# Kernel optimization log

Measured on AMD Instinct MI355X. Metric: run time of the kernel, lower is better.

## Reference

```python
import jax, jax.numpy as jnp
import numpy as np
from math import comb

K = 10
N_NODES = 100000
NUM_FEATURES = 512
HIDDEN = 256
NUM_CLASSES = 64
N_EDGES = 3200000


def setup_inputs() -> dict:
    key = jax.random.key(0)
    k = jax.random.split(key, 8)
    x = jax.random.normal(k[0], (N_NODES, NUM_FEATURES), dtype=jnp.float32)
    src = jax.random.randint(k[1], (N_EDGES,), 0, N_NODES, dtype=jnp.int32)
    dst = jax.random.randint(k[2], (N_EDGES,), 0, N_NODES, dtype=jnp.int32)
    # symmetrize so the sym-normalized Laplacian is well-defined (undirected graph)
    src2 = jnp.concatenate([src, dst])
    dst2 = jnp.concatenate([dst, src])
    edge_index = jnp.stack([src2, dst2], axis=0)  # [2, 2E]
    s1 = 1.0 / np.sqrt(NUM_FEATURES)
    s2 = 1.0 / np.sqrt(HIDDEN)
    W1 = jax.random.uniform(k[3], (NUM_FEATURES, HIDDEN), jnp.float32, -s1, s1)
    b1 = jax.random.uniform(k[4], (HIDDEN,), jnp.float32, -s1, s1)
    W2 = jax.random.uniform(k[5], (HIDDEN, NUM_CLASSES), jnp.float32, -s2, s2)
    b2 = jax.random.uniform(k[6], (NUM_CLASSES,), jnp.float32, -s2, s2)
    temp = jnp.ones((K + 1,), dtype=jnp.float32)  # reset_parameters fills with 1
    return {"x": x, "edge_index": edge_index, "W1": W1, "b1": b1, "W2": W2, "b2": b2, "temp": temp}


def bern_prop(h, src, dst, temp, num_nodes):
    # sym-normalized adjacency weights: w = d^{-1/2}[src] * d^{-1/2}[dst]
    deg = jax.ops.segment_sum(jnp.ones_like(src, dtype=h.dtype), src, num_segments=num_nodes)
    dis = jnp.where(deg > 0, jax.lax.rsqrt(jnp.maximum(deg, 1e-30)), 0.0)
    w = dis[src] * dis[dst]  # [E]

    def adj(v):  # A_hat @ v via gather + scatter-add (source_to_target flow)
        return jax.ops.segment_sum(w[:, None] * v[src], dst, num_segments=num_nodes)

    TEMP = jax.nn.relu(temp)
    coef = np.array([comb(K, i) / 2.0 ** K for i in range(K + 1)], dtype=np.float32)

    tmp = [h]
    for _ in range(K):  # (2I - L) h = h + A_hat h
        h = h + adj(h)
        tmp.append(h)
    out = coef[0] * TEMP[0] * tmp[K]
    for i in range(K):
        y = tmp[K - i - 1]
        for _ in range(i + 1):  # L y = y - A_hat y
            y = y - adj(y)
        out = out + coef[i + 1] * TEMP[i + 1] * y
    return out


def reference(x, edge_index, W1, b1, W2, b2, temp):
    # eval mode: dropout is identity
    h = jax.nn.relu(x @ W1 + b1)
    h = h @ W2 + b2  # [N, num_classes]
    src, dst = edge_index[0], edge_index[1]
    h = bern_prop(h, src, dst, temp, x.shape[0])
    return jax.nn.log_softmax(h, axis=1)
```

## Files before the change

### kernel.cpp

```cpp
#include <hip/hip_runtime.h>
#include <hip/hip_bf16.h>
#include <hip/hip_cooperative_groups.h>
#include <math.h>


#define KORD 10

namespace cg = cooperative_groups;

typedef __attribute__((ext_vector_type(8))) short bf16x8;
typedef __attribute__((ext_vector_type(4))) float f32x4;

typedef __attribute__((address_space(1))) const unsigned int* gas_t;
typedef __attribute__((address_space(3))) unsigned int* las_t;

static __device__ __forceinline__ void gll16(const void* g, void* l) {
    __builtin_amdgcn_global_load_lds((gas_t)g, (las_t)l, 16, 0, 0);
}

static __device__ __forceinline__ ushort f2bf(float f) {
    unsigned u = __float_as_uint(f);
    unsigned r = (u + 0x7fffu + ((u >> 16) & 1u)) >> 16;
    return (ushort)r;
}
static __device__ __forceinline__ float bf2f(ushort h) {
    return __uint_as_float(((unsigned)h) << 16);
}
static __device__ __forceinline__ uint pk2t(float a, float b) {
    return (__float_as_uint(a) >> 16) | (__float_as_uint(b) & 0xffff0000u);
}
static __device__ __forceinline__ bf16x8 mk8(uint a, uint b, uint c, uint d) {
    union { uint4 u; bf16x8 v; } x;
    x.u = make_uint4(a, b, c, d);
    return x.v;
}

__global__ void prep_all(const float* __restrict__ temp,
                         const float* __restrict__ W1, const float* __restrict__ W2,
                         float* __restrict__ acoef, int* __restrict__ flags,
                         ushort* __restrict__ w1b,
                         ushort* __restrict__ w2h, ushort* __restrict__ w2l)
{
    int tid = blockIdx.x * 256 + threadIdx.x;
    if (tid == 0) {
        int C[KORD + 1][KORD + 1];
        for (int n = 0; n <= KORD; ++n) {
            for (int k = 0; k <= KORD; ++k) C[n][k] = 0;
            C[n][0] = 1;
            for (int k = 1; k <= n; ++k)
                C[n][k] = C[n - 1][k - 1] + ((k <= n - 1) ? C[n - 1][k] : 0);
        }
        float a[KORD + 1];
        for (int j = 0; j <= KORD; ++j) a[j] = 0.f;
        for (int m = 0; m <= KORD; ++m) {
            float tm = temp[m];
            tm = tm > 0.f ? tm : 0.f;
            float cm = (float)C[KORD][m] / 1024.0f;
            for (int p = 0; p <= m; ++p)
                for (int q = 0; q <= KORD - m; ++q) {
                    int Mij = ((p & 1) ? -1 : 1) * C[m][p] * C[KORD - m][q];
                    a[p + q] += cm * tm * (float)Mij;
                }
        }
        for (int j = 0; j <= KORD; ++j) acoef[j] = a[j];
        int any = 0;
        for (int j = KORD; j >= 0; --j) {
            if (a[j] != 0.f) any = 1;
            flags[j] = any;
        }
    }
    if (tid < 512 * 256) {
        int j = tid & 7, lg = (tid >> 3) & 3, col = (tid >> 5) & 255, kt = tid >> 13;
        int k = kt * 32 + lg * 8 + j;
        w1b[tid] = f2bf(W1[k * 256 + col]);
    } else if (tid < 512 * 256 + 256 * 64) {
        int t2 = tid - 512 * 256;
        int j = t2 & 7, lg = (t2 >> 3) & 3, col = (t2 >> 5) & 63, ks = t2 >> 11;
        int k = ks * 32 + lg * 8 + j;
        float v = W2[k * 64 + col];
        ushort hi = f2bf(v);
        ushort lo = f2bf(v - bf2f(hi));
        w2h[t2] = hi; w2l[t2] = lo;
    }
}

__global__ __launch_bounds__(512, 4) void mlp_kernel(
    const float* __restrict__ x,
    const ushort* __restrict__ w1b,
    const ushort* __restrict__ w2h, const ushort* __restrict__ w2l,
    const float* __restrict__ b1, const float* __restrict__ b2,
    float* __restrict__ v0, float* __restrict__ out,
    const float* __restrict__ acoef, const int* __restrict__ flags, int N)
{
    __shared__ __align__(16) char sm[65536];

    const int t    = threadIdx.x;
    const int lane = t & 63;
    const int wid  = t >> 6;
    const int wm   = wid >> 2;
    const int wn   = wid & 3;
    const int l15  = lane & 15;
    const int lg   = lane >> 4;
    const int row0 = blockIdx.x * 128;
    const int wlds = (t >> 6) << 10;

    const int srow = t >> 3;
    const int skq  = t & 7;
    const int ssw  = (srow & 3) << 1;
    int gr0 = row0 + srow;      if (gr0 > N - 1) gr0 = N - 1;
    int gr1 = row0 + srow + 64; if (gr1 > N - 1) gr1 = N - 1;
    const float* gs0 = x + (size_t)gr0 * 512 + ((skq ^ ssw) << 2);
    const float* gs1 = x + (size_t)gr1 * 512 + ((skq ^ ssw) << 2);
    const char* w1g = (const char*)w1b;

    f32x4 acc[4][4];
#pragma unroll
    for (int i = 0; i < 4; ++i)
#pragma unroll
        for (int j = 0; j < 4; ++j) acc[i][j] = (f32x4)0.f;

    gll16(gs0,                 sm + wlds);
    gll16(gs1,                 sm + 8192 + wlds);
    gll16(w1g + t * 16,        sm + 32768 + wlds);
    gll16(w1g + 8192 + t * 16, sm + 40960 + wlds);
    __syncthreads();

#pragma unroll 2
    for (int kt = 0; kt < 16; ++kt) {
        if (kt < 15) {
            int ktn = kt + 1;
            char* An = sm + (ktn & 1) * 16384;
            char* Bn = sm + 32768 + (ktn & 1) * 16384;
            gll16(gs0 + ktn * 32,                       An + wlds);
            gll16(gs1 + ktn * 32,                       An + 8192 + wlds);
            gll16(w1g + ktn * 16384 + t * 16,           Bn + wlds);
            gll16(w1g + ktn * 16384 + 8192 + t * 16,    Bn + 8192 + wlds);
        }
        const char* Ac = sm + (kt & 1) * 16384;
        const char* Bc = sm + 32768 + (kt & 1) * 16384;
        bf16x8 Af[4];
#pragma unroll
        for (int mf = 0; mf < 4; ++mf) {
            int rowIdx = wm * 64 + mf * 16 + l15;
            int sw = (rowIdx & 3) << 1;
            const char* pa = Ac + rowIdx * 128 + (((2 * lg) ^ sw) << 4);
            float4 fa = *(const float4*)pa;
            float4 fb = *(const float4*)(pa + 16);
            Af[mf] = mk8(pk2t(fa.x, fa.y), pk2t(fa.z, fa.w),
                         pk2t(fb.x, fb.y), pk2t(fb.z, fb.w));
        }
#pragma unroll
        for (int nf = 0; nf < 4; ++nf) {
            bf16x8 B = *(const bf16x8*)(Bc + (wn * 64 + nf * 16 + l15) * 64 + lg * 16);
#pragma unroll
            for (int mf = 0; mf < 4; ++mf)
                acc[mf][nf] = __builtin_amdgcn_mfma_f32_16x16x32_bf16(Af[mf], B, acc[mf][nf], 0, 0, 0);
        }
        __syncthreads();
    }

    ushort* h1l = (ushort*)sm;
#pragma unroll
    for (int nf = 0; nf < 4; ++nf) {
        int col = wn * 64 + nf * 16 + l15;
        float bb = b1[col];
        int ks = col >> 5, lgw = (col >> 3) & 3, j = col & 7;
#pragma unroll
        for (int mf = 0; mf < 4; ++mf) {
            int g = wm * 4 + mf;
#pragma unroll
            for (int r = 0; r < 4; ++r) {
                float v = fmaxf(acc[mf][nf][r] + bb, 0.f);
                int l15w = lg * 4 + r;
                h1l[(((ks * 8 + g) * 64) + l15w * 4 + lgw) * 8 + j] = f2bf(v);
            }
        }
    }
    __syncthreads();

    f32x4 acc2[4];
#pragma unroll
    for (int i = 0; i < 4; ++i) acc2[i] = (f32x4)0.f;
#pragma unroll
    for (int ks = 0; ks < 8; ++ks) {
        bf16x8 A = *(const bf16x8*)&h1l[((ks * 8 + wid) * 64 + l15 * 4 + lg) * 8];
#pragma unroll
        for (int nf = 0; nf < 4; ++nf) {
            size_t bo = (size_t)ks * 2048 + (nf * 16 + l15) * 32 + (lg << 3);
            bf16x8 Bh = *(const bf16x8*)(w2h + bo);
            bf16x8 Bl = *(const bf16x8*)(w2l + bo);
            acc2[nf] = __builtin_amdgcn_mfma_f32_16x16x32_bf16(A, Bh, acc2[nf], 0, 0, 0);
            acc2[nf] = __builtin_amdgcn_mfma_f32_16x16x32_bf16(A, Bl, acc2[nf], 0, 0, 0);
        }
    }

    int flag1 = flags[1];
    float a0c = acoef[0];
    float z[4][4];
#pragma unroll
    for (int nf = 0; nf < 4; ++nf) {
        float bb = b2[nf * 16 + l15];
#pragma unroll
        for (int r = 0; r < 4; ++r) z[nf][r] = acc2[nf][r] + bb;
    }
    if (!flag1) {
#pragma unroll
        for (int r = 0; r < 4; ++r) {
            int row = row0 + wid * 16 + lg * 4 + r;
            float mx = fmaxf(fmaxf(z[0][r], z[1][r]), fmaxf(z[2][r], z[3][r]));
#pragma unroll
            for (int off = 1; off < 16; off <<= 1) mx = fmaxf(mx, __shfl_xor(mx, off, 64));
            float s = expf(z[0][r] - mx) + expf(z[1][r] - mx)
                    + expf(z[2][r] - mx) + expf(z[3][r] - mx);
#pragma unroll
            for (int off = 1; off < 16; off <<= 1) s += __shfl_xor(s, off, 64);
            float lns = logf(s);
            if (row < N) {
#pragma unroll
                for (int nf = 0; nf < 4; ++nf)
                    out[(size_t)row * 64 + nf * 16 + l15] = z[nf][r] - mx - lns;
            }
        }
    } else {
#pragma unroll
        for (int nf = 0; nf < 4; ++nf) {
            int col = nf * 16 + l15;
#pragma unroll
            for (int r = 0; r < 4; ++r) {
                int row = row0 + wid * 16 + lg * 4 + r;
                if (row < N) {
                    size_t o = (size_t)row * 64 + col;
                    v0[o] = z[nf][r];
                    out[o] = a0c * z[nf][r];
                }
            }
        }
    }
}

__global__ __launch_bounds__(256) void graph_coop(
    const int* __restrict__ src, const int* __restrict__ dst, int E, int N,
    int* __restrict__ degs, int* __restrict__ degd, int* __restrict__ cursor,
    int* __restrict__ rowp, int* __restrict__ csrs, float* __restrict__ csrw,
    float* __restrict__ v0, float* __restrict__ v1, float* __restrict__ out,
    const float* __restrict__ acoef, const int* __restrict__ flags)
{
    __shared__ int sums[256];
    if (!flags[1]) return;
    cg::grid_group grid = cg::this_grid();
    int gtid = blockIdx.x * 256 + threadIdx.x;
    int gstr = gridDim.x * 256;

    for (int i = gtid; i < N; i += gstr) { degs[i] = 0; degd[i] = 0; cursor[i] = 0; }
    grid.sync();
    for (int e = gtid; e < E; e += gstr) {
        atomicAdd(&degs[src[e]], 1);
        atomicAdd(&degd[dst[e]], 1);
    }
    grid.sync();
    if (blockIdx.x == 0) {
        int tid = threadIdx.x;
        int chunk = (N + 255) / 256;
        int s0 = tid * chunk;
        int s1 = s0 + chunk; if (s1 > N) s1 = N; if (s0 > N) s0 = N;
        int s = 0;
        for (int i = s0; i < s1; ++i) s += degd[i];
        sums[tid] = s;
        __syncthreads();
        for (int off = 1; off < 256; off <<= 1) {
            int v = (tid >= off) ? sums[tid - off] : 0;
            __syncthreads();
            sums[tid] += v;
            __syncthreads();
        }
        int run = sums[tid] - s;
        for (int i = s0; i < s1; ++i) { rowp[i] = run; run += degd[i]; }
        if (tid == 255) rowp[N] = sums[255];
    }
    grid.sync();
    for (int e = gtid; e < E; e += gstr) {
        int s = src[e], d = dst[e];
        int dgs = degs[s], dgd = degs[d];
        float ws_ = (dgs > 0 ? rsqrtf((float)dgs) : 0.f)
                  * (dgd > 0 ? rsqrtf((float)dgd) : 0.f);
        int slot = rowp[d] + atomicAdd(&cursor[d], 1);
        csrs[slot] = s;
        csrw[slot] = ws_;
    }
    grid.sync();
    const float* va = v0;
    float* vb = v1;
    int lane = threadIdx.x & 63;
    int grpbase = lane & 48;
    for (int j = 1; j <= KORD; ++j) {
        if (!flags[j]) break;
        float aj = acoef[j];
        for (int idx = gtid; idx < N * 16; idx += gstr) {
            int n = idx >> 4;
            int q = idx & 15;
            int beg = rowp[n], end = rowp[n + 1];
            float4 acc = make_float4(0.f, 0.f, 0.f, 0.f);
            for (int base = beg; base < end; base += 16) {
                int s = 0; float wvv = 0.f;
                int ii = base + q;
                if (ii < end) { s = csrs[ii]; wvv = csrw[ii]; }
                int m = end - base; if (m > 16) m = 16;
                for (int u = 0; u < m; ++u) {
                    int ss = __shfl(s, grpbase + u, 64);
                    float ww = __shfl(wvv, grpbase + u, 64);
                    float4 vv = *(const float4*)(va + ((long)ss << 6) + (q << 2));
                    acc.x += ww * vv.x; acc.y += ww * vv.y;
                    acc.z += ww * vv.z; acc.w += ww * vv.w;
                }
            }
            long o = ((long)n << 6) + (q << 2);
            *(float4*)(vb + o) = acc;
            float4 ov = *(const float4*)(out + o);
            ov.x += aj * acc.x; ov.y += aj * acc.y;
            ov.z += aj * acc.z; ov.w += aj * acc.w;
            *(float4*)(out + o) = ov;
        }
        grid.sync();
        float* tsw = vb; vb = (float*)va; va = tsw;
    }
    for (int idx = gtid; idx < N * 64; idx += gstr) {
        int n = idx >> 6;
        int c = idx & 63;
        float v = out[(long)n * 64 + c];
        float mx = v;
#pragma unroll
        for (int off = 32; off; off >>= 1) mx = fmaxf(mx, __shfl_xor(mx, off, 64));
        float e = expf(v - mx);
        float s = e;
#pragma unroll
        for (int off = 32; off; off >>= 1) s += __shfl_xor(s, off, 64);
        out[(long)n * 64 + c] = v - mx - logf(s);
    }
}

extern "C" void kernel_launch(void* const* d_in, const int* in_sizes, int n_in,
                              void* d_out, int out_size, void* d_ws, size_t ws_size,
                              hipStream_t stream)
{
    const float* x    = (const float*)d_in[0];
    const int*   ei   = (const int*)d_in[1];
    const float* W1   = (const float*)d_in[2];
    const float* b1   = (const float*)d_in[3];
    const float* W2   = (const float*)d_in[4];
    const float* b2   = (const float*)d_in[5];
    const float* temp = (const float*)d_in[6];

    int N = in_sizes[0] / 512;
    int E = in_sizes[1] / 2;
    const int* src = ei;
    const int* dst = ei + E;
    float* out = (float*)d_out;

    char* w = (char*)d_ws;
    auto alloc = [&](size_t bytes) {
        char* p = w;
        w += (bytes + 255) & ~(size_t)255;
        return p;
    };
    float* acoef  = (float*)alloc(64);
    int*   flags  = (int*)alloc(64);
    int*   degs   = (int*)alloc((size_t)N * 4);
    int*   degd   = (int*)alloc((size_t)N * 4);
    int*   cursor = (int*)alloc((size_t)N * 4);
    int*   rowp   = (int*)alloc((size_t)(N + 1) * 4);
    int*   csrs   = (int*)alloc((size_t)E * 4);
    float* csrw   = (float*)alloc((size_t)E * 4);
    ushort* w1b   = (ushort*)alloc(512 * 256 * 2);
    ushort* w2h   = (ushort*)alloc(256 * 64 * 2);
    ushort* w2l   = (ushort*)alloc(256 * 64 * 2);
    float* v0     = (float*)alloc((size_t)N * 64 * 4);
    float* v1     = (float*)alloc((size_t)N * 64 * 4);

    prep_all<<<576, 256, 0, stream>>>(temp, W1, W2, acoef, flags, w1b, w2h, w2l);

    int ntiles = (N + 127) / 128;
    mlp_kernel<<<ntiles, 512, 0, stream>>>(x, w1b, w2h, w2l, b1, b2, v0, out,
                                           acoef, flags, N);

    int Ei = E, Ni = N;
    void* cargs[] = {
        (void*)&src, (void*)&dst, (void*)&Ei, (void*)&Ni,
        (void*)&degs, (void*)&degd, (void*)&cursor, (void*)&rowp,
        (void*)&csrs, (void*)&csrw, (void*)&v0, (void*)&v1, (void*)&out,
        (void*)&acoef, (void*)&flags
    };
    hipLaunchCooperativeKernel((void*)graph_coop, dim3(1024), dim3(256),
                               cargs, 0, stream);
}
```

Baseline: 105.8 us.

## Shrink MLP block tile to 64 rows with 4 waves and wider per-wave N

Reworks the fused MLP kernel to use 64-row tiles with 256 threads (4 waves in a 2x2 arrangement, each covering 32 rows by 128 columns) instead of 128-row tiles with 512 threads. LDS drops to 48KB and the number of blocks doubles, which is meant to improve load balance and latency hiding across CUs. In exchange, each block reloads the full W1 tile for only half as many rows, doubling W1 traffic per row, and each wave keeps 16 accumulators instead of 16 with a different shape. The second GEMM stage's h1 layout is adjusted to match.

```diff
diff --git a/kernel.cpp b/kernel.cpp
--- a/kernel.cpp
+++ b/kernel.cpp
@@ -84,7 +84,7 @@
     }
 }
 
-__global__ __launch_bounds__(512, 4) void mlp_kernel(
+__global__ __launch_bounds__(256, 3) void mlp_kernel(
     const float* __restrict__ x,
     const ushort* __restrict__ w1b,
     const ushort* __restrict__ w2h, const ushort* __restrict__ w2l,
@@ -92,56 +92,60 @@
     float* __restrict__ v0, float* __restrict__ out,
     const float* __restrict__ acoef, const int* __restrict__ flags, int N)
 {
-    __shared__ __align__(16) char sm[65536];
+    __shared__ __align__(16) char sm[49152];
 
     const int t    = threadIdx.x;
     const int lane = t & 63;
     const int wid  = t >> 6;
-    const int wm   = wid >> 2;
-    const int wn   = wid & 3;
+    const int wm   = wid >> 1;
+    const int wn   = wid & 1;
     const int l15  = lane & 15;
     const int lg   = lane >> 4;
-    const int row0 = blockIdx.x * 128;
-    const int wlds = (t >> 6) << 10;
-
-    const int srow = t >> 3;
-    const int skq  = t & 7;
-    const int ssw  = (srow & 3) << 1;
-    int gr0 = row0 + srow;      if (gr0 > N - 1) gr0 = N - 1;
-    int gr1 = row0 + srow + 64; if (gr1 > N - 1) gr1 = N - 1;
-    const float* gs0 = x + (size_t)gr0 * 512 + ((skq ^ ssw) << 2);
-    const float* gs1 = x + (size_t)gr1 * 512 + ((skq ^ ssw) << 2);
+    const int row0 = blockIdx.x * 64;
+
+    const int arow0 = wid * 16 + (lane >> 3);
+    const int arow1 = arow0 + 8;
+    const int akq   = lane & 7;
+    int gr0 = row0 + arow0; if (gr0 > N - 1) gr0 = N - 1;
+    int gr1 = row0 + arow1; if (gr1 > N - 1) gr1 = N - 1;
+    const float* gsA0 = x + (size_t)gr0 * 512 + ((akq ^ ((arow0 & 3) << 1)) << 2);
+    const float* gsA1 = x + (size_t)gr1 * 512 + ((akq ^ ((arow1 & 3) << 1)) << 2);
     const char* w1g = (const char*)w1b;
-
-    f32x4 acc[4][4];
-#pragma unroll
-    for (int i = 0; i < 4; ++i)
-#pragma unroll
-        for (int j = 0; j < 4; ++j) acc[i][j] = (f32x4)0.f;
-
-    gll16(gs0,                 sm + wlds);
-    gll16(gs1,                 sm + 8192 + wlds);
-    gll16(w1g + t * 16,        sm + 32768 + wlds);
-    gll16(w1g + 8192 + t * 16, sm + 40960 + wlds);
+    const int aoff = wid * 2048;
+    const int boff = wid * 4096;
+
+    f32x4 acc[2][8];
+#pragma unroll
+    for (int i = 0; i < 2; ++i)
+#pragma unroll
+        for (int j = 0; j < 8; ++j) acc[i][j] = (f32x4)0.f;
+
+    gll16(gsA0, sm + aoff);
+    gll16(gsA1, sm + aoff + 1024);
+#pragma unroll
+    for (int c = 0; c < 4; ++c)
+        gll16(w1g + boff + c * 1024 + (lane << 4), sm + 16384 + boff + c * 1024);
     __syncthreads();
 
-#pragma unroll 2
+#pragma unroll
     for (int kt = 0; kt < 16; ++kt) {
         if (kt < 15) {
             int ktn = kt + 1;
-            char* An = sm + (ktn & 1) * 16384;
-            char* Bn = sm + 32768 + (ktn & 1) * 16384;
-            gll16(gs0 + ktn * 32,                       An + wlds);
-            gll16(gs1 + ktn * 32,                       An + 8192 + wlds);
-            gll16(w1g + ktn * 16384 + t * 16,           Bn + wlds);
-            gll16(w1g + ktn * 16384 + 8192 + t * 16,    Bn + 8192 + wlds);
-        }
-        const char* Ac = sm + (kt & 1) * 16384;
-        const char* Bc = sm + 32768 + (kt & 1) * 16384;
-        bf16x8 Af[4];
-#pragma unroll
-        for (int mf = 0; mf < 4; ++mf) {
-            int rowIdx = wm * 64 + mf * 16 + l15;
+            char* An = sm + (ktn & 1) * 8192;
+            char* Bn = sm + 16384 + (ktn & 1) * 16384;
+            gll16(gsA0 + ktn * 32, An + aoff);
+            gll16(gsA1 + ktn * 32, An + aoff + 1024);
+#pragma unroll
+            for (int c = 0; c < 4; ++c)
+                gll16(w1g + ktn * 16384 + boff + c * 1024 + (lane << 4),
+                      Bn + boff + c * 1024);
+        }
+        const char* Ac = sm + (kt & 1) * 8192;
+        const char* Bc = sm + 16384 + (kt & 1) * 16384;
+        bf16x8 Af[2];
+#pragma unroll
+        for (int mf = 0; mf < 2; ++mf) {
+            int rowIdx = wm * 32 + mf * 16 + l15;
             int sw = (rowIdx & 3) << 1;
             const char* pa = Ac + rowIdx * 128 + (((2 * lg) ^ sw) << 4);
             float4 fa = *(const float4*)pa;
@@ -150,29 +154,28 @@
                          pk2t(fb.x, fb.y), pk2t(fb.z, fb.w));
         }
 #pragma unroll
-        for (int nf = 0; nf < 4; ++nf) {
-            bf16x8 B = *(const bf16x8*)(Bc + (wn * 64 + nf * 16 + l15) * 64 + lg * 16);
-#pragma unroll
-            for (int mf = 0; mf < 4; ++mf)
-                acc[mf][nf] = __builtin_amdgcn_mfma_f32_16x16x32_bf16(Af[mf], B, acc[mf][nf], 0, 0, 0);
+        for (int nf = 0; nf < 8; ++nf) {
+            bf16x8 B = *(const bf16x8*)(Bc + (wn * 128 + nf * 16 + l15) * 64 + lg * 16);
+            acc[0][nf] = __builtin_amdgcn_mfma_f32_16x16x32_bf16(Af[0], B, acc[0][nf], 0, 0, 0);
+            acc[1][nf] = __builtin_amdgcn_mfma_f32_16x16x32_bf16(Af[1], B, acc[1][nf], 0, 0, 0);
         }
         __syncthreads();
     }
 
     ushort* h1l = (ushort*)sm;
 #pragma unroll
-    for (int nf = 0; nf < 4; ++nf) {
-        int col = wn * 64 + nf * 16 + l15;
+    for (int nf = 0; nf < 8; ++nf) {
+        int col = wn * 128 + nf * 16 + l15;
         float bb = b1[col];
         int ks = col >> 5, lgw = (col >> 3) & 3, j = col & 7;
 #pragma unroll
-        for (int mf = 0; mf < 4; ++mf) {
-            int g = wm * 4 + mf;
+        for (int mf = 0; mf < 2; ++mf) {
+            int g = wm * 2 + mf;
 #pragma unroll
             for (int r = 0; r < 4; ++r) {
                 float v = fmaxf(acc[mf][nf][r] + bb, 0.f);
                 int l15w = lg * 4 + r;
-                h1l[(((ks * 8 + g) * 64) + l15w * 4 + lgw) * 8 + j] = f2bf(v);
+                h1l[(((ks * 4 + g) * 64) + l15w * 4 + lgw) * 8 + j] = f2bf(v);
             }
         }
     }
@@ -183,7 +186,7 @@
     for (int i = 0; i < 4; ++i) acc2[i] = (f32x4)0.f;
 #pragma unroll
     for (int ks = 0; ks < 8; ++ks) {
-        bf16x8 A = *(const bf16x8*)&h1l[((ks * 8 + wid) * 64 + l15 * 4 + lg) * 8];
+        bf16x8 A = *(const bf16x8*)&h1l[((ks * 4 + wid) * 64 + l15 * 4 + lg) * 8];
 #pragma unroll
         for (int nf = 0; nf < 4; ++nf) {
             size_t bo = (size_t)ks * 2048 + (nf * 16 + l15) * 32 + (lg << 3);
@@ -378,8 +381,8 @@
 
     prep_all<<<576, 256, 0, stream>>>(temp, W1, W2, acoef, flags, w1b, w2h, w2l);
 
-    int ntiles = (N + 127) / 128;
-    mlp_kernel<<<ntiles, 512, 0, stream>>>(x, w1b, w2h, w2l, b1, b2, v0, out,
+    int ntiles = (N + 63) / 64;
+    mlp_kernel<<<ntiles, 256, 0, stream>>>(x, w1b, w2h, w2l, b1, b2, v0, out,
                                            acoef, flags, N);
 
     int Ei = E, Ni = N;
```

After: 112.4 us. 6.3% more time.

## Triple-buffer MLP GEMM loads with swizzled LDS layouts for A and B

Applied to the files above, without the earlier changes.

Changes the first-layer GEMM in the MLP kernel from double to triple buffering. Loads now run two k-tiles ahead, gated by explicit vmcnt waits and raw barriers instead of __syncthreads. The A-tile swizzle is widened to 8 ways, and W1's bf16 packing is XOR-swizzled in the prep kernel to cut LDS bank conflicts on the B reads. Shared memory grows to 96KB of dynamic LDS and the occupancy hint drops to 2 blocks per CU. This trades occupancy for deeper latency hiding, and the hand-counted vmcnt values must stay correct.

```diff
diff --git a/kernel.cpp b/kernel.cpp
--- a/kernel.cpp
+++ b/kernel.cpp
@@ -72,7 +72,8 @@
     if (tid < 512 * 256) {
         int j = tid & 7, lg = (tid >> 3) & 3, col = (tid >> 5) & 255, kt = tid >> 13;
         int k = kt * 32 + lg * 8 + j;
-        w1b[tid] = f2bf(W1[k * 256 + col]);
+        int pos = lg ^ (col & 3);
+        w1b[kt * 8192 + col * 32 + pos * 8 + j] = f2bf(W1[k * 256 + col]);
     } else if (tid < 512 * 256 + 256 * 64) {
         int t2 = tid - 512 * 256;
         int j = t2 & 7, lg = (t2 >> 3) & 3, col = (t2 >> 5) & 63, ks = t2 >> 11;
@@ -84,7 +85,7 @@
     }
 }
 
-__global__ __launch_bounds__(512, 4) void mlp_kernel(
+__global__ __launch_bounds__(512, 2) void mlp_kernel(
     const float* __restrict__ x,
     const ushort* __restrict__ w1b,
     const ushort* __restrict__ w2h, const ushort* __restrict__ w2l,
@@ -92,7 +93,7 @@
     float* __restrict__ v0, float* __restrict__ out,
     const float* __restrict__ acoef, const int* __restrict__ flags, int N)
 {
-    __shared__ __align__(16) char sm[65536];
+    extern __shared__ __align__(16) char sm[];
 
     const int t    = threadIdx.x;
     const int lane = t & 63;
@@ -102,16 +103,18 @@
     const int l15  = lane & 15;
     const int lg   = lane >> 4;
     const int row0 = blockIdx.x * 128;
-    const int wlds = (t >> 6) << 10;
-
-    const int srow = t >> 3;
-    const int skq  = t & 7;
-    const int ssw  = (srow & 3) << 1;
-    int gr0 = row0 + srow;      if (gr0 > N - 1) gr0 = N - 1;
-    int gr1 = row0 + srow + 64; if (gr1 > N - 1) gr1 = N - 1;
-    const float* gs0 = x + (size_t)gr0 * 512 + ((skq ^ ssw) << 2);
-    const float* gs1 = x + (size_t)gr1 * 512 + ((skq ^ ssw) << 2);
+
+    const int arow = t >> 3;
+    const int akq  = t & 7;
+    const int asw  = arow & 7;
+    int gr0 = row0 + arow;       if (gr0 > N - 1) gr0 = N - 1;
+    int gr1 = row0 + arow + 64;  if (gr1 > N - 1) gr1 = N - 1;
+    const float* gsA0 = x + (size_t)gr0 * 512 + ((akq ^ asw) << 2);
+    const float* gsA1 = x + (size_t)gr1 * 512 + ((akq ^ asw) << 2);
     const char* w1g = (const char*)w1b;
+    const char* gB0 = w1g + (size_t)wid * 1024 + ((size_t)lane << 4);
+    const char* gB1 = gB0 + 8192;
+    const int woff = wid * 1024;
 
     f32x4 acc[4][4];
 #pragma unroll
@@ -119,45 +122,66 @@
 #pragma unroll
         for (int j = 0; j < 4; ++j) acc[i][j] = (f32x4)0.f;
 
-    gll16(gs0,                 sm + wlds);
-    gll16(gs1,                 sm + 8192 + wlds);
-    gll16(w1g + t * 16,        sm + 32768 + wlds);
-    gll16(w1g + 8192 + t * 16, sm + 40960 + wlds);
+#define STAGE(KT, BUF) {                                                       \
+        char* Ad = sm + (BUF) * 16384;                                         \
+        char* Bd = sm + 49152 + (BUF) * 16384;                                 \
+        gll16(gsA0 + (size_t)(KT) * 32, Ad + woff);                            \
+        gll16(gsA1 + (size_t)(KT) * 32, Ad + 8192 + woff);                     \
+        gll16(gB0 + (size_t)(KT) * 16384, Bd + woff);                          \
+        gll16(gB1 + (size_t)(KT) * 16384, Bd + 8192 + woff);                   \
+    }
+
+#define COMPUTE(BUF) {                                                         \
+        const char* Ac = sm + (BUF) * 16384;                                   \
+        const char* Bc = sm + 49152 + (BUF) * 16384;                           \
+        bf16x8 Af[4];                                                          \
+        _Pragma("unroll")                                                      \
+        for (int mf = 0; mf < 4; ++mf) {                                       \
+            int rowIdx = wm * 64 + mf * 16 + l15;                              \
+            int sw = rowIdx & 7;                                               \
+            int u0 = (2 * lg) ^ sw;                                            \
+            const char* pr = Ac + rowIdx * 128;                                \
+            float4 fa = *(const float4*)(pr + (u0 << 4));                      \
+            float4 fb = *(const float4*)(pr + ((u0 ^ 1) << 4));                \
+            Af[mf] = mk8(pk2t(fa.x, fa.y), pk2t(fa.z, fa.w),                   \
+                         pk2t(fb.x, fb.y), pk2t(fb.z, fb.w));                  \
+        }                                                                      \
+        _Pragma("unroll")                                                      \
+        for (int nf = 0; nf < 4; ++nf) {                                       \
+            int col = wn * 64 + nf * 16 + l15;                                 \
+            const char* pb = Bc + col * 64 + ((lg ^ (col & 3)) << 4);          \
+            bf16x8 B = *(const bf16x8*)pb;                                     \
+            _Pragma("unroll")                                                  \
+            for (int mf = 0; mf < 4; ++mf)                                     \
+                acc[mf][nf] = __builtin_amdgcn_mfma_f32_16x16x32_bf16(         \
+                                  Af[mf], B, acc[mf][nf], 0, 0, 0);            \
+        }                                                                      \
+    }
+
+    STAGE(0, 0)
+    STAGE(1, 1)
+
+    int bc = 0;
+    for (int kt = 0; kt < 14; ++kt) {
+        int bn = bc + 2; if (bn >= 3) bn -= 3;
+        STAGE(kt + 2, bn)
+        asm volatile("s_waitcnt vmcnt(8)" ::: "memory");
+        __builtin_amdgcn_s_barrier();
+        COMPUTE(bc)
+        __builtin_amdgcn_s_barrier();
+        bc = (bc == 2) ? 0 : bc + 1;
+    }
+    asm volatile("s_waitcnt vmcnt(4)" ::: "memory");
+    __builtin_amdgcn_s_barrier();
+    COMPUTE(2)
+    __builtin_amdgcn_s_barrier();
+    asm volatile("s_waitcnt vmcnt(0)" ::: "memory");
+    __builtin_amdgcn_s_barrier();
+    COMPUTE(0)
     __syncthreads();
 
-#pragma unroll 2
-    for (int kt = 0; kt < 16; ++kt) {
-        if (kt < 15) {
-            int ktn = kt + 1;
-            char* An = sm + (ktn & 1) * 16384;
-            char* Bn = sm + 32768 + (ktn & 1) * 16384;
-            gll16(gs0 + ktn * 32,                       An + wlds);
-            gll16(gs1 + ktn * 32,                       An + 8192 + wlds);
-            gll16(w1g + ktn * 16384 + t * 16,           Bn + wlds);
-            gll16(w1g + ktn * 16384 + 8192 + t * 16,    Bn + 8192 + wlds);
-        }
-        const char* Ac = sm + (kt & 1) * 16384;
-        const char* Bc = sm + 32768 + (kt & 1) * 16384;
-        bf16x8 Af[4];
-#pragma unroll
-        for (int mf = 0; mf < 4; ++mf) {
-            int rowIdx = wm * 64 + mf * 16 + l15;
-            int sw = (rowIdx & 3) << 1;
-            const char* pa = Ac + rowIdx * 128 + (((2 * lg) ^ sw) << 4);
-            float4 fa = *(const float4*)pa;
-            float4 fb = *(const float4*)(pa + 16);
-            Af[mf] = mk8(pk2t(fa.x, fa.y), pk2t(fa.z, fa.w),
-                         pk2t(fb.x, fb.y), pk2t(fb.z, fb.w));
-        }
-#pragma unroll
-        for (int nf = 0; nf < 4; ++nf) {
-            bf16x8 B = *(const bf16x8*)(Bc + (wn * 64 + nf * 16 + l15) * 64 + lg * 16);
-#pragma unroll
-            for (int mf = 0; mf < 4; ++mf)
-                acc[mf][nf] = __builtin_amdgcn_mfma_f32_16x16x32_bf16(Af[mf], B, acc[mf][nf], 0, 0, 0);
-        }
-        __syncthreads();
-    }
+#undef STAGE
+#undef COMPUTE
 
     ushort* h1l = (ushort*)sm;
 #pragma unroll
@@ -376,11 +400,14 @@
     float* v0     = (float*)alloc((size_t)N * 64 * 4);
     float* v1     = (float*)alloc((size_t)N * 64 * 4);
 
+    hipFuncSetAttribute((const void*)mlp_kernel,
+                        hipFuncAttributeMaxDynamicSharedMemorySize, 98304);
+
     prep_all<<<576, 256, 0, stream>>>(temp, W1, W2, acoef, flags, w1b, w2h, w2l);
 
     int ntiles = (N + 127) / 128;
-    mlp_kernel<<<ntiles, 512, 0, stream>>>(x, w1b, w2h, w2l, b1, b2, v0, out,
-                                           acoef, flags, N);
+    mlp_kernel<<<ntiles, 512, 98304, stream>>>(x, w1b, w2h, w2l, b1, b2, v0, out,
+                                               acoef, flags, N);
 
     int Ei = E, Ni = N;
     void* cargs[] = {
```

Result: slower. 138.2 us (+30.7%).
